# Kernel optimization log

Hardware: AMD Instinct MI355X
Metric: run time of the kernel (lower is better)

## Reference

```python
import jax, jax.numpy as jnp
import numpy as np

N = 100000
E = 1600000
IN_DIM = 128
OUT_DIM = 128


def setup_inputs() -> dict:
    key = jax.random.key(0)
    k1, k2, k3, k4, k5 = jax.random.split(key, 5)
    x = jax.random.normal(k1, (N, IN_DIM), dtype=jnp.float32)
    edge_index = jax.random.randint(k2, (2, E), 0, N, dtype=jnp.int64)
    # LayerNorm affine params
    ln_w = jnp.ones((IN_DIM,), dtype=jnp.float32)
    ln_b = jnp.zeros((IN_DIM,), dtype=jnp.float32)
    # SAGEConv params: lin_l (neighbor agg, with bias), lin_r (root, no bias)
    s = 1.0 / np.sqrt(IN_DIM)
    W_l = jax.random.uniform(k3, (OUT_DIM, IN_DIM), dtype=jnp.float32, minval=-s, maxval=s)
    b_l = jax.random.uniform(k4, (OUT_DIM,), dtype=jnp.float32, minval=-s, maxval=s)
    W_r = jax.random.uniform(k5, (OUT_DIM, IN_DIM), dtype=jnp.float32, minval=-s, maxval=s)
    return {"x": x, "edge_index": edge_index, "ln_w": ln_w, "ln_b": ln_b,
            "W_l": W_l, "b_l": b_l, "W_r": W_r}


def _layer_norm(x, w, b, eps=1e-5):
    mu = jnp.mean(x, axis=-1, keepdims=True)
    var = jnp.mean(jnp.square(x - mu), axis=-1, keepdims=True)
    return (x - mu) * jax.lax.rsqrt(var + eps) * w + b


def reference(x, edge_index, ln_w, ln_b, W_l, b_l, W_r):
    # norm -> activation -> dropout(p=0, identity)
    h = jax.nn.relu(_layer_norm(x, ln_w, ln_b))  # [N, in_dim]
    src = edge_index[0]  # message sources (x_j)
    dst = edge_index[1]  # aggregation targets
    # mean aggregation of neighbor features onto target nodes
    agg = jax.ops.segment_sum(h[src], dst, num_segments=N)  # [N, in_dim]
    cnt = jax.ops.segment_sum(jnp.ones((E,), dtype=h.dtype), dst, num_segments=N)
    agg = agg / jnp.maximum(cnt, 1.0)[:, None]
    # SAGEConv: lin_l(agg) + lin_r(h)
    out = agg @ W_l.T + b_l + h @ W_r.T  # [N, out_dim]
    return out
```

## Files before the change

### kernel.cpp

```cpp
#include <hip/hip_runtime.h>

#define N_NODES 100000
#define E_EDGES 1600000
#define DIM     128

#define NB1     391
#define CHUNK   4096
#define NBINS   512
#define NBUCKET 391
#define NBH     (NBINS * NB1)
#define HS_BLOCKS 196

#define HB_OFF    0
#define WTB_OFF   25600000
#define OFFS_OFF  25665536
#define BHC_OFF   26065600
#define BH_OFF    26866432
#define BSUM_OFF  27667200
#define BIN_OFF   27668224
#define SRC_OFF   34068224
#define AGGB_OFF  40468224

typedef __attribute__((ext_vector_type(8))) short short8;
typedef __attribute__((ext_vector_type(4))) float floatx4;

__device__ __forceinline__ unsigned bf16pack(float a, float b) {
  unsigned ua = __float_as_uint(a); ua += 0x7fffu + ((ua >> 16) & 1u);
  unsigned ub = __float_as_uint(b); ub += 0x7fffu + ((ub >> 16) & 1u);
  return (ua >> 16) | (ub & 0xffff0000u);
}
__device__ __forceinline__ float2 bf16unpack(unsigned p) {
  return make_float2(__uint_as_float(p << 16), __uint_as_float(p & 0xffff0000u));
}

__global__ __launch_bounds__(256) void k_prep(const float* __restrict__ x,
                                              const float* __restrict__ lw,
                                              const float* __restrict__ lb,
                                              const float* __restrict__ Wl,
                                              const float* __restrict__ Wr,
                                              const int* __restrict__ ei,
                                              unsigned* __restrict__ hb,
                                              unsigned* __restrict__ wtb,
                                              int* __restrict__ bhc) {
  int gid = blockIdx.x * 256 + threadIdx.x;
  int t = threadIdx.x;

  {
    int row  = blockIdx.x * 4 + (t >> 6);
    int lane = t & 63;
    float2 v = ((const float2*)(x + (size_t)row * DIM))[lane];
    float s  = v.x + v.y;
    float sq = v.x * v.x + v.y * v.y;
    #pragma unroll
    for (int off = 32; off > 0; off >>= 1) {
      s  += __shfl_xor(s, off);
      sq += __shfl_xor(sq, off);
    }
    float mu  = s * (1.0f / 128.0f);
    float var = sq * (1.0f / 128.0f) - mu * mu;
    float rs  = rsqrtf(var + 1e-5f);
    float2 w = ((const float2*)lw)[lane];
    float2 b = ((const float2*)lb)[lane];
    float ox = fmaxf((v.x - mu) * rs * w.x + b.x, 0.0f);
    float oy = fmaxf((v.y - mu) * rs * w.y + b.y, 0.0f);
    hb[(size_t)row * 64 + lane] = bf16pack(ox, oy);
  }

  if (gid < 16384) {
    int j2 = gid & 3;
    int q  = (gid >> 2) & 3;
    int c  = (gid >> 4) & 127;
    int kb = gid >> 11;
    int k0 = kb * 32 + q * 8 + j2 * 2;
    int k1 = k0 + 1;
    float v0 = (k0 < 128) ? Wl[c * 128 + k0] : Wr[c * 128 + (k0 - 128)];
    float v1 = (k1 < 128) ? Wl[c * 128 + k1] : Wr[c * 128 + (k1 - 128)];
    wtb[gid] = bf16pack(v0, v1);
  }

  if (blockIdx.x < NB1) {
    __shared__ int h[NBINS];
    h[t] = 0; h[t + 256] = 0;
    __syncthreads();
    const int4* d4p = (const int4*)(ei + E_EDGES);
    #pragma unroll
    for (int u = 0; u < 4; ++u) {
      int i4 = blockIdx.x * (CHUNK / 4) + u * 256 + t;
      if (i4 < E_EDGES / 4) {
        int4 d = d4p[i4];
        atomicAdd(&h[d.x >> 8], 1);
        atomicAdd(&h[d.y >> 8], 1);
        atomicAdd(&h[d.z >> 8], 1);
        atomicAdd(&h[d.w >> 8], 1);
      }
    }
    __syncthreads();
    bhc[t * NB1 + blockIdx.x] = h[t];
    bhc[(t + 256) * NB1 + blockIdx.x] = h[t + 256];
  }
}

__global__ __launch_bounds__(256) void k_hscan1(const int* __restrict__ bhc,
                                                int* __restrict__ bh,
                                                int* __restrict__ bsum) {
  __shared__ int s[256];
  int t = threadIdx.x;
  int base = blockIdx.x * 1024 + t * 4;
  int a0 = (base + 0 < NBH) ? bhc[base + 0] : 0;
  int a1 = (base + 1 < NBH) ? bhc[base + 1] : 0;
  int a2 = (base + 2 < NBH) ? bhc[base + 2] : 0;
  int a3 = (base + 3 < NBH) ? bhc[base + 3] : 0;
  s[t] = a0 + a1 + a2 + a3;
  __syncthreads();
  #pragma unroll
  for (int off = 1; off < 256; off <<= 1) {
    int x = (t >= off) ? s[t - off] : 0;
    __syncthreads();
    s[t] += x;
    __syncthreads();
  }
  int excl = (t > 0) ? s[t - 1] : 0;
  if (t == 255) bsum[blockIdx.x] = s[255];
  if (base + 0 < NBH) bh[base + 0] = excl;
  if (base + 1 < NBH) bh[base + 1] = excl + a0;
  if (base + 2 < NBH) bh[base + 2] = excl + a0 + a1;
  if (base + 3 < NBH) bh[base + 3] = excl + a0 + a1 + a2;
}

__global__ __launch_bounds__(256) void k_binsort(const int* __restrict__ ei,
                                                 const int* __restrict__ bh,
                                                 const int* __restrict__ bhc,
                                                 const int* __restrict__ bsum,
                                                 int* __restrict__ binned) {
  __shared__ int stage[CHUNK];
  __shared__ int addr[CHUNK];
  __shared__ int hist[NBINS];
  __shared__ int ebase[NBINS];
  __shared__ int cur[NBINS];
  __shared__ int gbase[NBINS];
  __shared__ int s[256];
  __shared__ int bsc[256];
  int t  = threadIdx.x;
  int ch = blockIdx.x;

  s[t] = (t < HS_BLOCKS) ? bsum[t] : 0;
  __syncthreads();
  #pragma unroll
  for (int off = 1; off < 256; off <<= 1) {
    int xv = (t >= off) ? s[t - off] : 0;
    __syncthreads();
    s[t] += xv;
    __syncthreads();
  }
  bsc[t] = (t > 0) ? s[t - 1] : 0;
  __syncthreads();

  {
    int i0 = t * NB1 + ch;
    int i1 = (t + 256) * NB1 + ch;
    gbase[t]       = bh[i0] + bsc[i0 >> 10];
    gbase[t + 256] = bh[i1] + bsc[i1 >> 10];
    hist[t]        = bhc[i0];
    hist[t + 256]  = bhc[i1];
  }
  __syncthreads();

  int h0 = hist[2 * t], h1 = hist[2 * t + 1];
  s[t] = h0 + h1;
  __syncthreads();
  #pragma unroll
  for (int off = 1; off < 256; off <<= 1) {
    int xv = (t >= off) ? s[t - off] : 0;
    __syncthreads();
    s[t] += xv;
    __syncthreads();
  }
  int ex = (t > 0) ? s[t - 1] : 0;
  ebase[2 * t] = ex;
  ebase[2 * t + 1] = ex + h0;
  cur[2 * t] = ex;
  cur[2 * t + 1] = ex + h0;
  __syncthreads();

  const int4* s4p = (const int4*)ei;
  const int4* d4p = (const int4*)(ei + E_EDGES);

  #pragma unroll
  for (int u = 0; u < 4; ++u) {
    int i4 = ch * (CHUNK / 4) + u * 256 + t;
    if (i4 < E_EDGES / 4) {
      int4 sv = s4p[i4];
      int4 dv = d4p[i4];
      {
        int bin = dv.x >> 8; int pos = atomicAdd(&cur[bin], 1);
        stage[pos] = sv.x | ((dv.x & 255) << 20);
        addr[pos]  = gbase[bin] + (pos - ebase[bin]);
      }
      {
        int bin = dv.y >> 8; int pos = atomicAdd(&cur[bin], 1);
        stage[pos] = sv.y | ((dv.y & 255) << 20);
        addr[pos]  = gbase[bin] + (pos - ebase[bin]);
      }
      {
        int bin = dv.z >> 8; int pos = atomicAdd(&cur[bin], 1);
        stage[pos] = sv.z | ((dv.z & 255) << 20);
        addr[pos]  = gbase[bin] + (pos - ebase[bin]);
      }
      {
        int bin = dv.w >> 8; int pos = atomicAdd(&cur[bin], 1);
        stage[pos] = sv.w | ((dv.w & 255) << 20);
        addr[pos]  = gbase[bin] + (pos - ebase[bin]);
      }
    }
  }
  __syncthreads();

  int cbase = ch * CHUNK;
  int cnt = E_EDGES - cbase;
  if (cnt > CHUNK) cnt = CHUNK;
  for (int i = t; i < cnt; i += 256)
    binned[addr[i]] = stage[i];
}

__global__ __launch_bounds__(256) void k_csr(const int* __restrict__ bh,
                                             const int* __restrict__ bsum,
                                             const int* __restrict__ binned,
                                             int* __restrict__ offs,
                                             int* __restrict__ srcidx) {
  __shared__ int h[256];
  __shared__ int s[256];
  __shared__ int cur[256];
  __shared__ int bsc[256];
  int t = threadIdx.x;
  int bin = blockIdx.x;

  s[t] = (t < HS_BLOCKS) ? bsum[t] : 0;
  __syncthreads();
  #pragma unroll
  for (int off = 1; off < 256; off <<= 1) {
    int xv = (t >= off) ? s[t - off] : 0;
    __syncthreads();
    s[t] += xv;
    __syncthreads();
  }
  bsc[t] = (t > 0) ? s[t - 1] : 0;
  __syncthreads();

  int i0 = bin * NB1, i1 = (bin + 1) * NB1;
  int base = bh[i0] + bsc[i0 >> 10];
  int end  = (bin + 1 < NBINS) ? (bh[i1] + bsc[i1 >> 10]) : E_EDGES;

  h[t] = 0;
  __syncthreads();
  for (int i = base + t; i < end; i += 256)
    atomicAdd(&h[(binned[i] >> 20) & 255], 1);
  __syncthreads();
  s[t] = h[t];
  __syncthreads();
  #pragma unroll
  for (int off = 1; off < 256; off <<= 1) {
    int x = (t >= off) ? s[t - off] : 0;
    __syncthreads();
    s[t] += x;
    __syncthreads();
  }
  int excl = (t > 0) ? s[t - 1] : 0;
  cur[t] = excl;
  int node = bin * 256 + t;
  if (node < N_NODES) offs[node] = base + excl;
  if (node == N_NODES) offs[N_NODES] = E_EDGES;
  __syncthreads();
  for (int i = base + t; i < end; i += 256) {
    int p = binned[i];
    int r = atomicAdd(&cur[(p >> 20) & 255], 1);
    srcidx[base + r] = p & 0xFFFFF;
  }
}

__global__ __launch_bounds__(256) void k_gather(const unsigned* __restrict__ hb,
                                                const int* __restrict__ offs,
                                                const int* __restrict__ srcidx,
                                                unsigned* __restrict__ aggb) {
  int wave = threadIdx.x >> 6;
  int lane = threadIdx.x & 63;
  int n0 = blockIdx.x * 8 + wave * 2;
  int n1 = n0 + 1;
  int b0 = __builtin_amdgcn_readfirstlane(offs[n0]);
  int e0 = __builtin_amdgcn_readfirstlane(offs[n0 + 1]);
  int b1 = __builtin_amdgcn_readfirstlane(offs[n1]);
  int e1 = __builtin_amdgcn_readfirstlane(offs[n1 + 1]);
  int m0 = e0 - b0, m1 = e1 - b1;
  int c  = (m0 < m1 ? m0 : m1) & ~7;

  float ax0 = 0.0f, ay0 = 0.0f, ax1 = 0.0f, ay1 = 0.0f;

  for (int j = 0; j < c; j += 8) {
    unsigned p0[8], p1[8];
    #pragma unroll
    for (int i = 0; i < 8; ++i) {
      int s0 = srcidx[b0 + j + i];
      int s1 = srcidx[b1 + j + i];
      p0[i] = hb[(size_t)s0 * 64 + lane];
      p1[i] = hb[(size_t)s1 * 64 + lane];
    }
    #pragma unroll
    for (int i = 0; i < 8; ++i) {
      float2 v0 = bf16unpack(p0[i]);
      float2 v1 = bf16unpack(p1[i]);
      ax0 += v0.x; ay0 += v0.y;
      ax1 += v1.x; ay1 += v1.y;
    }
  }
  for (int j = b0 + c; j < e0; ) {
    int rem = e0 - j;
    if (rem >= 8) {
      unsigned p[8];
      #pragma unroll
      for (int i = 0; i < 8; ++i) p[i] = hb[(size_t)srcidx[j + i] * 64 + lane];
      #pragma unroll
      for (int i = 0; i < 8; ++i) { float2 v = bf16unpack(p[i]); ax0 += v.x; ay0 += v.y; }
      j += 8;
    } else {
      float2 v = bf16unpack(hb[(size_t)srcidx[j] * 64 + lane]);
      ax0 += v.x; ay0 += v.y;
      ++j;
    }
  }
  for (int j = b1 + c; j < e1; ) {
    int rem = e1 - j;
    if (rem >= 8) {
      unsigned p[8];
      #pragma unroll
      for (int i = 0; i < 8; ++i) p[i] = hb[(size_t)srcidx[j + i] * 64 + lane];
      #pragma unroll
      for (int i = 0; i < 8; ++i) { float2 v = bf16unpack(p[i]); ax1 += v.x; ay1 += v.y; }
      j += 8;
    } else {
      float2 v = bf16unpack(hb[(size_t)srcidx[j] * 64 + lane]);
      ax1 += v.x; ay1 += v.y;
      ++j;
    }
  }

  float inv0 = 1.0f / fmaxf((float)m0, 1.0f);
  float inv1 = 1.0f / fmaxf((float)m1, 1.0f);
  aggb[(size_t)n0 * 64 + lane] = bf16pack(ax0 * inv0, ay0 * inv0);
  aggb[(size_t)n1 * 64 + lane] = bf16pack(ax1 * inv1, ay1 * inv1);
}

__global__ __launch_bounds__(256) void k_gemm(const unsigned* __restrict__ aggb,
                                              const unsigned* __restrict__ hb,
                                              const unsigned* __restrict__ wtb,
                                              const float* __restrict__ bl,
                                              float* __restrict__ out) {
  int wave = threadIdx.x >> 6;
  int lane = threadIdx.x & 63;
  int m = lane & 15;
  int q = lane >> 4;
  int r0 = blockIdx.x * 64 + wave * 16;
  int rowA = r0 + m;
  if (rowA > N_NODES - 1) rowA = N_NODES - 1;

  const uint4* ar = (const uint4*)(aggb + (size_t)rowA * 64);
  const uint4* hr = (const uint4*)(hb + (size_t)rowA * 64);
  short8 afrag[8];
  #pragma unroll
  for (int kb = 0; kb < 4; ++kb) {
    uint4 u = ar[kb * 4 + q];
    afrag[kb] = *(short8*)&u;
  }
  #pragma unroll
  for (int kb = 0; kb < 4; ++kb) {
    uint4 u = hr[kb * 4 + q];
    afrag[kb + 4] = *(short8*)&u;
  }

  const uint4* b4 = (const uint4*)wtb;
  #pragma unroll
  for (int ct = 0; ct < 8; ++ct) {
    int c = ct * 16 + m;
    floatx4 acc = {0.0f, 0.0f, 0.0f, 0.0f};
    #pragma unroll
    for (int kb = 0; kb < 8; ++kb) {
      uint4 u = b4[kb * 512 + c * 4 + q];
      short8 bfrag = *(short8*)&u;
      acc = __builtin_amdgcn_mfma_f32_16x16x32_bf16(afrag[kb], bfrag, acc, 0, 0, 0);
    }
    float bias = bl[c];
    #pragma unroll
    for (int reg = 0; reg < 4; ++reg) {
      int r = r0 + q * 4 + reg;
      if (r < N_NODES) out[(size_t)r * DIM + c] = acc[reg] + bias;
    }
  }
}

extern "C" void kernel_launch(void* const* d_in, const int* in_sizes, int n_in,
                              void* d_out, int out_size, void* d_ws, size_t ws_size,
                              hipStream_t stream) {
  const float* x  = (const float*)d_in[0];
  const int*   ei = (const int*)d_in[1];
  const float* lw = (const float*)d_in[2];
  const float* lb = (const float*)d_in[3];
  const float* Wl = (const float*)d_in[4];
  const float* bl = (const float*)d_in[5];
  const float* Wr = (const float*)d_in[6];
  float* out = (float*)d_out;

  char* ws = (char*)d_ws;
  unsigned* hb     = (unsigned*)(ws + HB_OFF);
  unsigned* wtb    = (unsigned*)(ws + WTB_OFF);
  int*      offs   = (int*)(ws + OFFS_OFF);
  int*      bhc    = (int*)(ws + BHC_OFF);
  int*      bh     = (int*)(ws + BH_OFF);
  int*      bsum   = (int*)(ws + BSUM_OFF);
  int*      binned = (int*)(ws + BIN_OFF);
  int*      srcidx = (int*)(ws + SRC_OFF);
  unsigned* aggb   = (unsigned*)(ws + AGGB_OFF);

  k_prep<<<N_NODES / 4, 256, 0, stream>>>(x, lw, lb, Wl, Wr, ei, hb, wtb, bhc);
  k_hscan1<<<HS_BLOCKS, 256, 0, stream>>>(bhc, bh, bsum);
  k_binsort<<<NB1, 256, 0, stream>>>(ei, bh, bhc, bsum, binned);
  k_csr<<<NBUCKET, 256, 0, stream>>>(bh, bsum, binned, offs, srcidx);
  k_gather<<<N_NODES / 8, 256, 0, stream>>>(hb, offs, srcidx, aggb);
  k_gemm<<<(N_NODES + 63) / 64, 256, 0, stream>>>(aggb, hb, wtb, bl, out);
}
```

Baseline: 251.8 us.

## Stage CSR bin edges in LDS and sort neighbor lists per node

```diff
diff --git a/kernel.cpp b/kernel.cpp
--- a/kernel.cpp
+++ b/kernel.cpp
@@ -10,6 +10,7 @@
 #define NBUCKET 391
 #define NBH     (NBINS * NB1)
 #define HS_BLOCKS 196
+#define LDSCAP  5120
 
 #define HB_OFF    0
 #define WTB_OFF   25600000
@@ -231,6 +232,8 @@
   __shared__ int s[256];
   __shared__ int cur[256];
   __shared__ int bsc[256];
+  __shared__ int stg[LDSCAP];
+  __shared__ int stg2[LDSCAP];
   int t = threadIdx.x;
   int bin = blockIdx.x;
 
@@ -249,31 +252,77 @@
   int i0 = bin * NB1, i1 = (bin + 1) * NB1;
   int base = bh[i0] + bsc[i0 >> 10];
   int end  = (bin + 1 < NBINS) ? (bh[i1] + bsc[i1 >> 10]) : E_EDGES;
+  int cnt  = end - base;
 
   h[t] = 0;
   __syncthreads();
-  for (int i = base + t; i < end; i += 256)
-    atomicAdd(&h[(binned[i] >> 20) & 255], 1);
-  __syncthreads();
-  s[t] = h[t];
-  __syncthreads();
-  #pragma unroll
-  for (int off = 1; off < 256; off <<= 1) {
-    int x = (t >= off) ? s[t - off] : 0;
-    __syncthreads();
-    s[t] += x;
-    __syncthreads();
-  }
-  int excl = (t > 0) ? s[t - 1] : 0;
-  cur[t] = excl;
-  int node = bin * 256 + t;
-  if (node < N_NODES) offs[node] = base + excl;
-  if (node == N_NODES) offs[N_NODES] = E_EDGES;
-  __syncthreads();
-  for (int i = base + t; i < end; i += 256) {
-    int p = binned[i];
-    int r = atomicAdd(&cur[(p >> 20) & 255], 1);
-    srcidx[base + r] = p & 0xFFFFF;
+
+  if (cnt <= LDSCAP) {
+    for (int i = t; i < cnt; i += 256) stg[i] = binned[base + i];
+    __syncthreads();
+    for (int i = t; i < cnt; i += 256)
+      atomicAdd(&h[(stg[i] >> 20) & 255], 1);
+    __syncthreads();
+    s[t] = h[t];
+    __syncthreads();
+    #pragma unroll
+    for (int off = 1; off < 256; off <<= 1) {
+      int x = (t >= off) ? s[t - off] : 0;
+      __syncthreads();
+      s[t] += x;
+      __syncthreads();
+    }
+    int excl = (t > 0) ? s[t - 1] : 0;
+    cur[t] = excl;
+    int node = bin * 256 + t;
+    if (node < N_NODES) offs[node] = base + excl;
+    if (node == N_NODES) offs[N_NODES] = E_EDGES;
+    __syncthreads();
+    for (int i = t; i < cnt; i += 256) {
+      int p = stg[i];
+      int r = atomicAdd(&cur[(p >> 20) & 255], 1);
+      stg2[r] = p & 0xFFFFF;
+    }
+    __syncthreads();
+    {
+      int len = h[t];
+      int beg = excl;
+      for (int a = 1; a < len; ++a) {
+        int key = stg2[beg + a];
+        int b = a - 1;
+        while (b >= 0 && stg2[beg + b] > key) {
+          stg2[beg + b + 1] = stg2[beg + b];
+          --b;
+        }
+        stg2[beg + b + 1] = key;
+      }
+    }
+    __syncthreads();
+    for (int i = t; i < cnt; i += 256) srcidx[base + i] = stg2[i];
+  } else {
+    for (int i = base + t; i < end; i += 256)
+      atomicAdd(&h[(binned[i] >> 20) & 255], 1);
+    __syncthreads();
+    s[t] = h[t];
+    __syncthreads();
+    #pragma unroll
+    for (int off = 1; off < 256; off <<= 1) {
+      int x = (t >= off) ? s[t - off] : 0;
+      __syncthreads();
+      s[t] += x;
+      __syncthreads();
+    }
+    int excl = (t > 0) ? s[t - 1] : 0;
+    cur[t] = excl;
+    int node = bin * 256 + t;
+    if (node < N_NODES) offs[node] = base + excl;
+    if (node == N_NODES) offs[N_NODES] = E_EDGES;
+    __syncthreads();
+    for (int i = base + t; i < end; i += 256) {
+      int p = binned[i];
+      int r = atomicAdd(&cur[(p >> 20) & 255], 1);
+      srcidx[base + r] = p & 0xFFFFF;
+    }
   }
 }
 
```

Result: slower. 292.4 us (+16.1%).

## Drop global histogram scan kernel; binsort writes chunk-local, CSR computes bucket offsets

Applied to the files above, without the earlier changes.

```diff
diff --git a/kernel.cpp b/kernel.cpp
--- a/kernel.cpp
+++ b/kernel.cpp
@@ -9,17 +9,15 @@
 #define NBINS   512
 #define NBUCKET 391
 #define NBH     (NBINS * NB1)
-#define HS_BLOCKS 196
 
 #define HB_OFF    0
 #define WTB_OFF   25600000
 #define OFFS_OFF  25665536
 #define BHC_OFF   26065600
-#define BH_OFF    26866432
-#define BSUM_OFF  27667200
-#define BIN_OFF   27668224
-#define SRC_OFF   34068224
-#define AGGB_OFF  40468224
+#define EBG_OFF   26866432
+#define BIN_OFF   27667264
+#define SRC_OFF   34067264
+#define AGGB_OFF  40467264
 
 typedef __attribute__((ext_vector_type(8))) short short8;
 typedef __attribute__((ext_vector_type(4))) float floatx4;
@@ -100,69 +98,20 @@
   }
 }
 
-__global__ __launch_bounds__(256) void k_hscan1(const int* __restrict__ bhc,
-                                                int* __restrict__ bh,
-                                                int* __restrict__ bsum) {
-  __shared__ int s[256];
-  int t = threadIdx.x;
-  int base = blockIdx.x * 1024 + t * 4;
-  int a0 = (base + 0 < NBH) ? bhc[base + 0] : 0;
-  int a1 = (base + 1 < NBH) ? bhc[base + 1] : 0;
-  int a2 = (base + 2 < NBH) ? bhc[base + 2] : 0;
-  int a3 = (base + 3 < NBH) ? bhc[base + 3] : 0;
-  s[t] = a0 + a1 + a2 + a3;
-  __syncthreads();
-  #pragma unroll
-  for (int off = 1; off < 256; off <<= 1) {
-    int x = (t >= off) ? s[t - off] : 0;
-    __syncthreads();
-    s[t] += x;
-    __syncthreads();
-  }
-  int excl = (t > 0) ? s[t - 1] : 0;
-  if (t == 255) bsum[blockIdx.x] = s[255];
-  if (base + 0 < NBH) bh[base + 0] = excl;
-  if (base + 1 < NBH) bh[base + 1] = excl + a0;
-  if (base + 2 < NBH) bh[base + 2] = excl + a0 + a1;
-  if (base + 3 < NBH) bh[base + 3] = excl + a0 + a1 + a2;
-}
-
 __global__ __launch_bounds__(256) void k_binsort(const int* __restrict__ ei,
-                                                 const int* __restrict__ bh,
                                                  const int* __restrict__ bhc,
-                                                 const int* __restrict__ bsum,
-                                                 int* __restrict__ binned) {
+                                                 int* __restrict__ binned,
+                                                 int* __restrict__ ebg) {
   __shared__ int stage[CHUNK];
-  __shared__ int addr[CHUNK];
   __shared__ int hist[NBINS];
   __shared__ int ebase[NBINS];
   __shared__ int cur[NBINS];
-  __shared__ int gbase[NBINS];
   __shared__ int s[256];
-  __shared__ int bsc[256];
   int t  = threadIdx.x;
   int ch = blockIdx.x;
 
-  s[t] = (t < HS_BLOCKS) ? bsum[t] : 0;
-  __syncthreads();
-  #pragma unroll
-  for (int off = 1; off < 256; off <<= 1) {
-    int xv = (t >= off) ? s[t - off] : 0;
-    __syncthreads();
-    s[t] += xv;
-    __syncthreads();
-  }
-  bsc[t] = (t > 0) ? s[t - 1] : 0;
-  __syncthreads();
-
-  {
-    int i0 = t * NB1 + ch;
-    int i1 = (t + 256) * NB1 + ch;
-    gbase[t]       = bh[i0] + bsc[i0 >> 10];
-    gbase[t + 256] = bh[i1] + bsc[i1 >> 10];
-    hist[t]        = bhc[i0];
-    hist[t + 256]  = bhc[i1];
-  }
+  hist[t]       = bhc[t * NB1 + ch];
+  hist[t + 256] = bhc[(t + 256) * NB1 + ch];
   __syncthreads();
 
   int h0 = hist[2 * t], h1 = hist[2 * t + 1];
@@ -180,6 +129,8 @@
   ebase[2 * t + 1] = ex + h0;
   cur[2 * t] = ex;
   cur[2 * t + 1] = ex + h0;
+  ebg[(2 * t) * NB1 + ch]     = ex;
+  ebg[(2 * t + 1) * NB1 + ch] = ex + h0;
   __syncthreads();
 
   const int4* s4p = (const int4*)ei;
@@ -194,22 +145,18 @@
       {
         int bin = dv.x >> 8; int pos = atomicAdd(&cur[bin], 1);
         stage[pos] = sv.x | ((dv.x & 255) << 20);
-        addr[pos]  = gbase[bin] + (pos - ebase[bin]);
       }
       {
         int bin = dv.y >> 8; int pos = atomicAdd(&cur[bin], 1);
         stage[pos] = sv.y | ((dv.y & 255) << 20);
-        addr[pos]  = gbase[bin] + (pos - ebase[bin]);
       }
       {
         int bin = dv.z >> 8; int pos = atomicAdd(&cur[bin], 1);
         stage[pos] = sv.z | ((dv.z & 255) << 20);
-        addr[pos]  = gbase[bin] + (pos - ebase[bin]);
       }
       {
         int bin = dv.w >> 8; int pos = atomicAdd(&cur[bin], 1);
         stage[pos] = sv.w | ((dv.w & 255) << 20);
-        addr[pos]  = gbase[bin] + (pos - ebase[bin]);
       }
     }
   }
@@ -219,42 +166,53 @@
   int cnt = E_EDGES - cbase;
   if (cnt > CHUNK) cnt = CHUNK;
   for (int i = t; i < cnt; i += 256)
-    binned[addr[i]] = stage[i];
-}
-
-__global__ __launch_bounds__(256) void k_csr(const int* __restrict__ bh,
-                                             const int* __restrict__ bsum,
+    binned[cbase + i] = stage[i];
+}
+
+__global__ __launch_bounds__(256) void k_csr(const int* __restrict__ bhc,
+                                             const int* __restrict__ ebg,
                                              const int* __restrict__ binned,
                                              int* __restrict__ offs,
                                              int* __restrict__ srcidx) {
   __shared__ int h[256];
   __shared__ int s[256];
   __shared__ int cur[256];
-  __shared__ int bsc[256];
+  __shared__ int bhcRow[NB1];
+  __shared__ int ebgRow[NB1];
+  __shared__ int baseSh;
   int t = threadIdx.x;
-  int bin = blockIdx.x;
-
-  s[t] = (t < HS_BLOCKS) ? bsum[t] : 0;
-  __syncthreads();
-  #pragma unroll
-  for (int off = 1; off < 256; off <<= 1) {
-    int xv = (t >= off) ? s[t - off] : 0;
-    __syncthreads();
-    s[t] += xv;
-    __syncthreads();
-  }
-  bsc[t] = (t > 0) ? s[t - 1] : 0;
-  __syncthreads();
-
-  int i0 = bin * NB1, i1 = (bin + 1) * NB1;
-  int base = bh[i0] + bsc[i0 >> 10];
-  int end  = (bin + 1 < NBINS) ? (bh[i1] + bsc[i1 >> 10]) : E_EDGES;
-
+  int b = blockIdx.x;
+
+  for (int i = t; i < NB1; i += 256) {
+    bhcRow[i] = bhc[b * NB1 + i];
+    ebgRow[i] = ebg[b * NB1 + i];
+  }
   h[t] = 0;
   __syncthreads();
-  for (int i = base + t; i < end; i += 256)
-    atomicAdd(&h[(binned[i] >> 20) & 255], 1);
-  __syncthreads();
+
+  {
+    int p = 0;
+    for (int i = t; i < NB1; i += 256) p += ebgRow[i];
+    s[t] = p;
+    __syncthreads();
+    #pragma unroll
+    for (int off = 128; off > 0; off >>= 1) {
+      if (t < off) s[t] += s[t + off];
+      __syncthreads();
+    }
+    if (t == 0) baseSh = s[0];
+    __syncthreads();
+  }
+  int base = baseSh;
+
+  for (int ch = t; ch < NB1; ch += 256) {
+    int st = ch * CHUNK + ebgRow[ch];
+    int len = bhcRow[ch];
+    for (int k = 0; k < len; ++k)
+      atomicAdd(&h[(binned[st + k] >> 20) & 255], 1);
+  }
+  __syncthreads();
+
   s[t] = h[t];
   __syncthreads();
   #pragma unroll
@@ -266,14 +224,19 @@
   }
   int excl = (t > 0) ? s[t - 1] : 0;
   cur[t] = excl;
-  int node = bin * 256 + t;
+  int node = b * 256 + t;
   if (node < N_NODES) offs[node] = base + excl;
   if (node == N_NODES) offs[N_NODES] = E_EDGES;
   __syncthreads();
-  for (int i = base + t; i < end; i += 256) {
-    int p = binned[i];
-    int r = atomicAdd(&cur[(p >> 20) & 255], 1);
-    srcidx[base + r] = p & 0xFFFFF;
+
+  for (int ch = t; ch < NB1; ch += 256) {
+    int st = ch * CHUNK + ebgRow[ch];
+    int len = bhcRow[ch];
+    for (int k = 0; k < len; ++k) {
+      int p = binned[st + k];
+      int r = atomicAdd(&cur[(p >> 20) & 255], 1);
+      srcidx[base + r] = p & 0xFFFFF;
+    }
   }
 }
 
@@ -412,16 +375,14 @@
   unsigned* wtb    = (unsigned*)(ws + WTB_OFF);
   int*      offs   = (int*)(ws + OFFS_OFF);
   int*      bhc    = (int*)(ws + BHC_OFF);
-  int*      bh     = (int*)(ws + BH_OFF);
-  int*      bsum   = (int*)(ws + BSUM_OFF);
+  int*      ebg    = (int*)(ws + EBG_OFF);
   int*      binned = (int*)(ws + BIN_OFF);
   int*      srcidx = (int*)(ws + SRC_OFF);
   unsigned* aggb   = (unsigned*)(ws + AGGB_OFF);
 
   k_prep<<<N_NODES / 4, 256, 0, stream>>>(x, lw, lb, Wl, Wr, ei, hb, wtb, bhc);
-  k_hscan1<<<HS_BLOCKS, 256, 0, stream>>>(bhc, bh, bsum);
-  k_binsort<<<NB1, 256, 0, stream>>>(ei, bh, bhc, bsum, binned);
-  k_csr<<<NBUCKET, 256, 0, stream>>>(bh, bsum, binned, offs, srcidx);
+  k_binsort<<<NB1, 256, 0, stream>>>(ei, bhc, binned, ebg);
+  k_csr<<<NBUCKET, 256, 0, stream>>>(bhc, ebg, binned, offs, srcidx);
   k_gather<<<N_NODES / 8, 256, 0, stream>>>(hb, offs, srcidx, aggb);
   k_gemm<<<(N_NODES + 63) / 64, 256, 0, stream>>>(aggb, hb, wtb, bl, out);
 }
```

After: 254.4 us. Within noise of the previous version (+1.1%).
